# Performance work log

Measured on AMD Instinct MI355X. Metric: run time of the kernel, lower is better.

The kernel has to match this reference:

```python
import jax, jax.numpy as jnp
import numpy as np

B, D_IN, D_Z, D_H, D_T, D_REC = 8192, 1024, 256, 256, 16, 256


def _softplus_beta(x, beta):
    # torch F.softplus(x, beta) = (1/beta) * log(1 + exp(beta*x))
    return jax.nn.softplus(beta * x) / beta


def setup_inputs() -> dict:
    key = jax.random.key(0)
    ks = jax.random.split(key, 17)
    w = lambda k, o, i: jax.random.normal(k, (o, i), jnp.float32) * (1.0 / np.sqrt(i))
    return {
        "I_t": jax.random.uniform(ks[0], (B, D_IN), jnp.float32),
        "h_m_1": jax.random.uniform(ks[1], (B, D_H), jnp.float32),
        "z_m_1": jax.random.uniform(ks[2], (B, D_Z), jnp.float32),
        "theta_m_1": jax.random.normal(ks[3], (B, D_T), jnp.float32),
        "eps_z": jax.random.normal(ks[4], (B, D_Z), jnp.float32),
        "eps_zhat": jax.random.normal(ks[5], (B, D_Z), jnp.float32),
        "W_post_mu": w(ks[6], D_Z, D_IN),
        "W_post_lv": w(ks[7], D_Z, D_IN),
        "W_z2h": w(ks[8], D_H, D_Z),
        "W_h2h": w(ks[9], D_H, D_H),
        "W_prior_mu": w(ks[10], D_Z, D_H),
        "W_prior_lv": w(ks[11], D_Z, D_H),
        "W_i2t": w(ks[12], D_T, D_IN),
        "W_vip2t": w(ks[13], D_T, D_Z),
        "W_t2z": w(ks[14], D_Z, D_T),
        "W_rec1": w(ks[15], D_REC, D_Z),
        "W_rec2": w(ks[16], D_IN, D_REC),
    }


def reference(I_t, h_m_1, z_m_1, theta_m_1, eps_z, eps_zhat,
              W_post_mu, W_post_lv, W_z2h, W_h2h, W_prior_mu, W_prior_lv,
              W_i2t, W_vip2t, W_t2z, W_rec1, W_rec2):
    relu = jax.nn.relu
    # prior pathway (perception_only=True branch)
    mu_p = relu(h_m_1 @ W_prior_mu.T)                       # [B, D_Z]
    sigma_p = _softplus_beta(h_m_1 @ W_prior_lv.T, 1.2)     # [B, D_Z]
    # theta dynamics; vip_to_theta has Positive parametrization -> relu(W)
    theta_h = (0.5 * theta_m_1 + 0.1 * (I_t @ W_i2t.T)
               - jax.lax.stop_gradient(sigma_p) @ relu(W_vip2t).T)  # [B, D_T]
    theta = 0.001 * _softplus_beta(theta_h, 0.5)
    # posterior + reparameterized sample
    mu_q = relu(I_t @ W_post_mu.T)
    sigma_q = relu(I_t @ W_post_lv.T)
    raw_z = jnp.clip(mu_q + eps_z * sigma_q, 0.0, 1.0)
    thresholds = 10.0 * (theta @ relu(W_t2z).T)             # Positive parametrization
    z = relu(raw_z - thresholds)                            # [B, D_Z]
    # reconstruction (two bias-free linears + sigmoid)
    I_hat = jax.nn.sigmoid((z @ W_rec1.T) @ W_rec2.T)       # [B, D_IN]
    # higher-state update and prior sample
    h = relu(z_m_1 @ W_z2h.T + h_m_1 @ W_h2h.T)             # [B, D_H]
    z_hat = mu_p + eps_zhat * sigma_p                       # [B, D_Z]
    # losses (as in torch forward)
    spatial = jnp.mean((I_t - I_hat) ** 2)
    temporal = jnp.mean((jax.lax.stop_gradient(z) - z_hat) ** 2)
    energy = jnp.mean(jnp.abs(z))
    return (I_hat, z, h, z_hat, spatial, temporal, energy)
```

## Files before the change

### kernel.cpp

```cpp
#include <hip/hip_runtime.h>
#include <math.h>

#define BB 8192
#define DIN 1024
#define DZ 256
#define DH 256
#define DT 16
#define DREC 256

#define OFF_IHAT 0
#define OFF_Z    (BB * DIN)
#define OFF_H    (OFF_Z + BB * DZ)
#define OFF_ZHAT (OFF_H + BB * DH)
#define OFF_SCAL (OFF_ZHAT + BB * DZ)

#define WS_HBF   0
#define WS_ZM1   2097152
#define WS_W     4194304
#define W_PM  (WS_W + 0)
#define W_PL  (W_PM + 262144)
#define W_Z2H (W_PL + 262144)
#define W_H2H (W_Z2H + 65536)
#define W_PRM (W_H2H + 65536)
#define W_PRL (W_PRM + 65536)
#define W_I2T (W_PRL + 65536)
#define W_VIP (W_I2T + 16384)
#define W_R1  (W_VIP + 4096)
#define W_R2  (W_R1 + 65536)
#define WS_ENDW  (W_R2 + 262144)
#define WS_SIGMA WS_ENDW
#define WS_ZBF   (WS_SIGMA + 2097152)
#define WS_R1BF  (WS_ZBF + 2097152)

typedef unsigned short u16;
typedef __attribute__((ext_vector_type(8))) unsigned short u16x8;
typedef __attribute__((ext_vector_type(8))) __bf16 bf16x8;
typedef __attribute__((ext_vector_type(4))) float f32x4;

#define MFMA __builtin_amdgcn_mfma_f32_16x16x32_bf16

__device__ inline u16 f2bf(float f) {
  unsigned u = __builtin_bit_cast(unsigned, f);
  u += 0x7fff + ((u >> 16) & 1);
  return (u16)(u >> 16);
}
__device__ inline float softplus_stable(float y) {
  return (y > 20.f) ? y : log1pf(expf(y));
}
__device__ inline bf16x8 gf(const u16* p) {
  return __builtin_bit_cast(bf16x8, *(const u16x8*)p);
}
__device__ inline f32x4 fzero() { return (f32x4){0.f, 0.f, 0.f, 0.f}; }

__device__ inline float block_sum256(float v, float* rbuf) {
#pragma unroll
  for (int off = 32; off > 0; off >>= 1) v += __shfl_down(v, off, 64);
  __syncthreads();
  if ((threadIdx.x & 63) == 0) rbuf[threadIdx.x >> 6] = v;
  __syncthreads();
  return rbuf[0] + rbuf[1] + rbuf[2] + rbuf[3];
}

__device__ inline void decode4(int id, int rows, int& row0, int& col0) {
  int xcd = id & 7, t = id >> 3;
  col0 = (t & 3) * 64;
  row0 = ((t >> 2) * 8 + xcd) * rows;
}

__device__ inline void dmaA32(u16* tile, const u16* __restrict__ gsrc,
                              int row0, int ldk, int k0) {
  const int lane = threadIdx.x & 63, w = threadIdx.x >> 6;
  int rb = w * 8;
  int r = rb + (lane >> 3);
  int gl = (lane & 7) ^ (r & 7);
  const u16* src = gsrc + (size_t)(row0 + r) * ldk + k0 + gl * 8;
  u16* dst = tile + rb * 64;
  __builtin_amdgcn_global_load_lds(
      (const __attribute__((address_space(1))) unsigned int*)(const void*)src,
      (__attribute__((address_space(3))) unsigned int*)(void*)dst, 16, 0, 0);
}
__device__ inline void dmaB64(u16* tile, const u16* __restrict__ gsrc,
                              int row0, int ldk, int k0) {
  const int lane = threadIdx.x & 63, w = threadIdx.x >> 6;
#pragma unroll
  for (int c = 0; c < 2; ++c) {
    int rb = w * 16 + c * 8;
    int r = rb + (lane >> 3);
    int gl = (lane & 7) ^ (r & 7);
    const u16* src = gsrc + (size_t)(row0 + r) * ldk + k0 + gl * 8;
    u16* dst = tile + rb * 64;
    __builtin_amdgcn_global_load_lds(
        (const __attribute__((address_space(1))) unsigned int*)(const void*)src,
        (__attribute__((address_space(3))) unsigned int*)(void*)dst, 16, 0, 0);
  }
}
__device__ inline void dma16(u16* tile, const u16* __restrict__ gsrc, int ldk,
                             int k0) {
  const int lane = threadIdx.x & 63, w = threadIdx.x >> 6;
  if (w < 2) {
    int rb = w * 8;
    int r = rb + (lane >> 3);
    int gl = (lane & 7) ^ (r & 7);
    const u16* src = gsrc + (size_t)r * ldk + k0 + gl * 8;
    u16* dst = tile + rb * 64;
    __builtin_amdgcn_global_load_lds(
        (const __attribute__((address_space(1))) unsigned int*)(const void*)src,
        (__attribute__((address_space(3))) unsigned int*)(void*)dst, 16, 0, 0);
  }
}
__device__ inline bf16x8 rd(const u16* tile, int r, int gl) {
  return gf(tile + r * 64 + ((gl ^ (r & 7)) * 8));
}

__global__ __launch_bounds__(256) void k_cvt(
    const float* __restrict__ I_t, const float* __restrict__ h_m_1,
    const float* __restrict__ z_m_1, const float* __restrict__ Wpm,
    const float* __restrict__ Wpl, const float* __restrict__ Wz2h,
    const float* __restrict__ Wh2h, const float* __restrict__ Wprm,
    const float* __restrict__ Wprl, const float* __restrict__ Wi2t,
    const float* __restrict__ Wv, const float* __restrict__ Wr1,
    const float* __restrict__ Wr2, u16* __restrict__ dstI,
    u16* __restrict__ dstW) {
  const int S1 = 8388608, S2 = 10485760, S3 = 12582912, S4 = 12845056,
            S5 = 13107200, S6 = 13172736, S7 = 13238272, S8 = 13303808,
            S9 = 13369344, S10 = 13385728, S11 = 13389824, S12 = 13455360,
            S13 = 13717504;
  int nchunk = S13 / 8;
  for (int c = blockIdx.x * 256 + threadIdx.x; c < nchunk;
       c += gridDim.x * 256) {
    int f = c * 8;
    const float* src;
    float scale = 1.f;
    bool nrelu = false;
    u16* dst;
    if (f < S1) {
      src = I_t + f;
      dst = dstI + f;
    } else {
      dst = dstW + (f - S1);
      if (f < S2)       src = h_m_1 + (f - S1);
      else if (f < S3)  src = z_m_1 + (f - S2);
      else if (f < S4)  src = Wpm + (f - S3);
      else if (f < S5)  src = Wpl + (f - S4);
      else if (f < S6)  src = Wz2h + (f - S5);
      else if (f < S7)  src = Wh2h + (f - S6);
      else if (f < S8)  src = Wprm + (f - S7);
      else if (f < S9)  src = Wprl + (f - S8);
      else if (f < S10) { src = Wi2t + (f - S9);  scale = 0.1f; }
      else if (f < S11) { src = Wv + (f - S10);   nrelu = true; }
      else if (f < S12) src = Wr1 + (f - S11);
      else              src = Wr2 + (f - S12);
    }
    float4 v0 = *(const float4*)(src);
    float4 v1 = *(const float4*)(src + 4);
    float vals[8] = {v0.x, v0.y, v0.z, v0.w, v1.x, v1.y, v1.z, v1.w};
    u16x8 o;
#pragma unroll
    for (int j = 0; j < 8; ++j) {
      float x = vals[j];
      x = nrelu ? -fmaxf(x, 0.f) : x * scale;
      o[j] = f2bf(x);
    }
    *(u16x8*)(dst) = o;
  }
}

__global__ __launch_bounds__(256, 4) void k_hp(
    const u16* __restrict__ h_bf, const u16* __restrict__ zm1,
    const u16* __restrict__ Wh2h, const u16* __restrict__ Wprm,
    const u16* __restrict__ Wprl, const u16* __restrict__ Wz2h,
    const float* __restrict__ eps_zhat, float* __restrict__ h_out,
    float* __restrict__ zhat_out, u16* __restrict__ sigma_bf) {
  __shared__ __align__(16) u16 smem[2048 + 3 * 4096];
  u16* As = smem;
  u16* B0s = smem + 2048;
  u16* B1s = B0s + 4096;
  u16* B2s = B1s + 4096;
  const int tid = threadIdx.x, lane = tid & 63, w = tid >> 6;
  const int frow = lane & 15, fq = lane >> 4;
  const int wr = w & 1, wc = w >> 1;
  int row0, col0;
  decode4(blockIdx.x, 32, row0, col0);

  f32x4 ah[2], am[2], as_[2];
#pragma unroll
  for (int i = 0; i < 2; ++i) { ah[i] = fzero(); am[i] = fzero(); as_[i] = fzero(); }

  for (int k0 = 0; k0 < DH; k0 += 64) {
    __syncthreads();
    dmaA32(As, h_bf, row0, DH, k0);
    dmaB64(B0s, Wh2h, col0, DH, k0);
    dmaB64(B1s, Wprm, col0, DH, k0);
    dmaB64(B2s, Wprl, col0, DH, k0);
    __syncthreads();
#pragma unroll
    for (int ks = 0; ks < 2; ++ks) {
      bf16x8 a = rd(As, wr * 16 + frow, ks * 4 + fq);
#pragma unroll
      for (int ni = 0; ni < 2; ++ni) {
        int br = wc * 32 + ni * 16 + frow;
        ah[ni]  = MFMA(a, rd(B0s, br, ks * 4 + fq), ah[ni], 0, 0, 0);
        am[ni]  = MFMA(a, rd(B1s, br, ks * 4 + fq), am[ni], 0, 0, 0);
        as_[ni] = MFMA(a, rd(B2s, br, ks * 4 + fq), as_[ni], 0, 0, 0);
      }
    }
  }
  for (int k0 = 0; k0 < DZ; k0 += 64) {
    __syncthreads();
    dmaA32(As, zm1, row0, DZ, k0);
    dmaB64(B0s, Wz2h, col0, DZ, k0);
    __syncthreads();
#pragma unroll
    for (int ks = 0; ks < 2; ++ks) {
      bf16x8 a = rd(As, wr * 16 + frow, ks * 4 + fq);
#pragma unroll
      for (int ni = 0; ni < 2; ++ni)
        ah[ni] = MFMA(a, rd(B0s, wc * 32 + ni * 16 + frow, ks * 4 + fq),
                      ah[ni], 0, 0, 0);
    }
  }
  __syncthreads();
  float* ht = (float*)smem;
  float* mt = (float*)(smem + 4224);
  float* st = (float*)(smem + 8448);
#pragma unroll
  for (int ni = 0; ni < 2; ++ni)
#pragma unroll
    for (int r = 0; r < 4; ++r) {
      int lr = wr * 16 + fq * 4 + r;
      int ln = wc * 32 + ni * 16 + frow;
      ht[lr * 66 + ln] = fmaxf(ah[ni][r], 0.f);
      mt[lr * 66 + ln] = fmaxf(am[ni][r], 0.f);
      st[lr * 66 + ln] = softplus_stable(1.2f * as_[ni][r]) * (1.f / 1.2f);
    }
  __syncthreads();
  {
    int lr2 = tid >> 3, c0 = (tid & 7) * 8;
    int m2 = row0 + lr2;
    float h8[8], mu8[8], sg8[8];
#pragma unroll
    for (int j = 0; j < 8; ++j) {
      h8[j] = ht[lr2 * 66 + c0 + j];
      mu8[j] = mt[lr2 * 66 + c0 + j];
      sg8[j] = st[lr2 * 66 + c0 + j];
    }
    float* hp = h_out + (size_t)m2 * DH + col0 + c0;
    *(float4*)hp = make_float4(h8[0], h8[1], h8[2], h8[3]);
    *(float4*)(hp + 4) = make_float4(h8[4], h8[5], h8[6], h8[7]);
    const float* ep = eps_zhat + (size_t)m2 * DZ + col0 + c0;
    float4 e0 = ((const float4*)ep)[0], e1 = ((const float4*)ep)[1];
    float e8[8] = {e0.x, e0.y, e0.z, e0.w, e1.x, e1.y, e1.z, e1.w};
    float zh8[8];
    u16x8 sb;
#pragma unroll
    for (int j = 0; j < 8; ++j) {
      zh8[j] = mu8[j] + e8[j] * sg8[j];
      sb[j] = f2bf(sg8[j]);
    }
    float* zp = zhat_out + (size_t)m2 * DZ + col0 + c0;
    *(float4*)zp = make_float4(zh8[0], zh8[1], zh8[2], zh8[3]);
    *(float4*)(zp + 4) = make_float4(zh8[4], zh8[5], zh8[6], zh8[7]);
    *(u16x8*)(sigma_bf + (size_t)m2 * DZ + col0 + c0) = sb;
  }
}

__global__ __launch_bounds__(256, 4) void k_post(
    const u16* __restrict__ I_bf, const u16* __restrict__ Wpm,
    const u16* __restrict__ Wpl, const u16* __restrict__ Wi2t,
    const u16* __restrict__ Wv, const u16* __restrict__ sigma_bf,
    const float* __restrict__ theta_m_1, const float* __restrict__ W_t2z,
    const float* __restrict__ eps_z, const float* __restrict__ zhat,
    float* __restrict__ z_out, u16* __restrict__ z_bf,
    float* __restrict__ scal) {
  __shared__ __align__(16) u16 smem[2048 + 4096 + 4096 + 1024];
  u16* As = smem;
  u16* B0s = smem + 2048;
  u16* B1s = B0s + 4096;
  u16* Bts = B1s + 4096;
  __shared__ float th_s[32 * 17];
  __shared__ float wt_s[64 * 17];
  __shared__ float rbuf[4];
  const int tid = threadIdx.x, lane = tid & 63, w = tid >> 6;
  const int frow = lane & 15, fq = lane >> 4;
  const int wr = w & 1, wc = w >> 1;
  int row0, col0;
  decode4(blockIdx.x, 32, row0, col0);

  f32x4 accm[2], accs[2], acct = fzero();
#pragma unroll
  for (int i = 0; i < 2; ++i) { accm[i] = fzero(); accs[i] = fzero(); }

  for (int k0 = 0; k0 < DIN; k0 += 64) {
    __syncthreads();
    dmaA32(As, I_bf, row0, DIN, k0);
    dmaB64(B0s, Wpm, col0, DIN, k0);
    dmaB64(B1s, Wpl, col0, DIN, k0);
    dma16(Bts, Wi2t, DIN, k0);
    __syncthreads();
#pragma unroll
    for (int ks = 0; ks < 2; ++ks) {
      bf16x8 a = rd(As, wr * 16 + frow, ks * 4 + fq);
#pragma unroll
      for (int ni = 0; ni < 2; ++ni) {
        int br = wc * 32 + ni * 16 + frow;
        accm[ni] = MFMA(a, rd(B0s, br, ks * 4 + fq), accm[ni], 0, 0, 0);
        accs[ni] = MFMA(a, rd(B1s, br, ks * 4 + fq), accs[ni], 0, 0, 0);
      }
      acct = MFMA(a, rd(Bts, frow, ks * 4 + fq), acct, 0, 0, 0);
    }
  }
  for (int k0 = 0; k0 < DZ; k0 += 64) {
    __syncthreads();
    dmaA32(As, sigma_bf, row0, DZ, k0);
    dma16(Bts, Wv, DZ, k0);
    __syncthreads();
#pragma unroll
    for (int ks = 0; ks < 2; ++ks)
      acct = MFMA(rd(As, wr * 16 + frow, ks * 4 + fq),
                  rd(Bts, frow, ks * 4 + fq), acct, 0, 0, 0);
  }
  __syncthreads();
  if (wc == 0) {
#pragma unroll
    for (int r = 0; r < 4; ++r) {
      int lr = wr * 16 + fq * 4 + r;
      float th = 0.5f * theta_m_1[(size_t)(row0 + lr) * DT + frow] + acct[r];
      th_s[lr * 17 + frow] = 0.002f * softplus_stable(0.5f * th);
    }
  }
  for (int idx = tid; idx < 64 * 16; idx += 256) {
    int n = idx >> 4, j = idx & 15;
    wt_s[n * 17 + j] = 10.f * fmaxf(W_t2z[(col0 + n) * DT + j], 0.f);
  }
  __syncthreads();
  float* zt = (float*)B0s;
#pragma unroll
  for (int ni = 0; ni < 2; ++ni)
#pragma unroll
    for (int r = 0; r < 4; ++r) {
      int lr = wr * 16 + fq * 4 + r;
      int ln = wc * 32 + ni * 16 + frow;
      int m = row0 + lr;
      float mu = fmaxf(accm[ni][r], 0.f);
      float sq = fmaxf(accs[ni][r], 0.f);
      float raw = mu + eps_z[(size_t)m * DZ + col0 + ln] * sq;
      raw = fminf(fmaxf(raw, 0.f), 1.f);
      float thr = 0.f;
#pragma unroll
      for (int j = 0; j < 16; ++j)
        thr = fmaf(th_s[lr * 17 + j], wt_s[ln * 17 + j], thr);
      zt[lr * 66 + ln] = fmaxf(raw - thr, 0.f);
    }
  __syncthreads();
  float tsum = 0.f, esum = 0.f;
  {
    int lr2 = tid >> 3, c0 = (tid & 7) * 8;
    int m2 = row0 + lr2;
    float z8[8];
#pragma unroll
    for (int j = 0; j < 8; ++j) z8[j] = zt[lr2 * 66 + c0 + j];
    float* zp = z_out + (size_t)m2 * DZ + col0 + c0;
    *(float4*)zp = make_float4(z8[0], z8[1], z8[2], z8[3]);
    *(float4*)(zp + 4) = make_float4(z8[4], z8[5], z8[6], z8[7]);
    u16x8 zb;
#pragma unroll
    for (int j = 0; j < 8; ++j) zb[j] = f2bf(z8[j]);
    *(u16x8*)(z_bf + (size_t)m2 * DZ + col0 + c0) = zb;
    const float* zhp = zhat + (size_t)m2 * DZ + col0 + c0;
    float4 h0 = ((const float4*)zhp)[0], h1 = ((const float4*)zhp)[1];
    float zh8[8] = {h0.x, h0.y, h0.z, h0.w, h1.x, h1.y, h1.z, h1.w};
#pragma unroll
    for (int j = 0; j < 8; ++j) {
      float d = z8[j] - zh8[j];
      tsum += d * d;
      esum += z8[j];
    }
  }
  float t = block_sum256(tsum, rbuf);
  if (tid == 0) atomicAdd(scal + 1, t * (1.f / ((float)BB * DZ)));
  float e = block_sum256(esum, rbuf);
  if (tid == 0) atomicAdd(scal + 2, e * (1.f / ((float)BB * DZ)));
}

__global__ __launch_bounds__(256, 4) void k_rec1(const u16* __restrict__ z_bf,
                                                 const u16* __restrict__ Wr1,
                                                 u16* __restrict__ r1_bf) {
  __shared__ __align__(16) u16 smem[2048 + 4096];
  u16* As = smem;
  u16* B0s = smem + 2048;
  const int tid = threadIdx.x, lane = tid & 63, w = tid >> 6;
  const int frow = lane & 15, fq = lane >> 4;
  const int wr = w & 1, wc = w >> 1;
  int row0, col0;
  decode4(blockIdx.x, 32, row0, col0);
  f32x4 acc[2] = {fzero(), fzero()};
  for (int k0 = 0; k0 < DZ; k0 += 64) {
    __syncthreads();
    dmaA32(As, z_bf, row0, DZ, k0);
    dmaB64(B0s, Wr1, col0, DZ, k0);
    __syncthreads();
#pragma unroll
    for (int ks = 0; ks < 2; ++ks) {
      bf16x8 a = rd(As, wr * 16 + frow, ks * 4 + fq);
#pragma unroll
      for (int ni = 0; ni < 2; ++ni)
        acc[ni] = MFMA(a, rd(B0s, wc * 32 + ni * 16 + frow, ks * 4 + fq),
                       acc[ni], 0, 0, 0);
    }
  }
  __syncthreads();
  float* rt = (float*)smem;
#pragma unroll
  for (int ni = 0; ni < 2; ++ni)
#pragma unroll
    for (int r = 0; r < 4; ++r) {
      int lr = wr * 16 + fq * 4 + r;
      int ln = wc * 32 + ni * 16 + frow;
      rt[lr * 66 + ln] = acc[ni][r];
    }
  __syncthreads();
  {
    int lr2 = tid >> 3, c0 = (tid & 7) * 8;
    int m2 = row0 + lr2;
    u16x8 rb;
#pragma unroll
    for (int j = 0; j < 8; ++j) rb[j] = f2bf(rt[lr2 * 66 + c0 + j]);
    *(u16x8*)(r1_bf + (size_t)m2 * DREC + col0 + c0) = rb;
  }
}

__global__ __launch_bounds__(256, 4) void k_rec2(const u16* __restrict__ r1_bf,
                                                 const u16* __restrict__ Wr2,
                                                 const float* __restrict__ I_t,
                                                 float* __restrict__ ihat_out,
                                                 float* __restrict__ scal) {
  __shared__ __align__(16) u16 smem[4096 + 4096];
  u16* As = smem;
  u16* B0s = smem + 4096;
  __shared__ float rbuf[4];
  const int tid = threadIdx.x, lane = tid & 63, w = tid >> 6;
  const int frow = lane & 15, fq = lane >> 4;
  int row0, col0;
  {
    int id = blockIdx.x;
    int xcd = id & 7, t = id >> 3;
    col0 = (t & 15) * 64;
    row0 = ((t >> 4) * 8 + xcd) * 64;
  }
  f32x4 acc[4] = {fzero(), fzero(), fzero(), fzero()};
  for (int k0 = 0; k0 < DREC; k0 += 64) {
    __syncthreads();
    dmaB64(As, r1_bf, row0, DREC, k0);
    dmaB64(B0s, Wr2, col0, DREC, k0);
    __syncthreads();
#pragma unroll
    for (int ks = 0; ks < 2; ++ks) {
      bf16x8 a = rd(As, w * 16 + frow, ks * 4 + fq);
#pragma unroll
      for (int ni = 0; ni < 4; ++ni)
        acc[ni] = MFMA(a, rd(B0s, ni * 16 + frow, ks * 4 + fq), acc[ni], 0, 0, 0);
    }
  }
  float lsum = 0.f;
  float* it = (float*)smem;
#pragma unroll 1
  for (int p = 0; p < 2; ++p) {
    __syncthreads();
    if ((w >> 1) == p) {
#pragma unroll
      for (int ni = 0; ni < 4; ++ni)
#pragma unroll
        for (int r = 0; r < 4; ++r) {
          int lrl = (w & 1) * 16 + fq * 4 + r;
          int ln = ni * 16 + frow;
          it[lrl * 66 + ln] = 1.f / (1.f + expf(-acc[ni][r]));
        }
    }
    __syncthreads();
    int lr2 = tid >> 3, c0 = (tid & 7) * 8;
    int m2 = row0 + p * 32 + lr2;
    float i8[8];
#pragma unroll
    for (int j = 0; j < 8; ++j) i8[j] = it[lr2 * 66 + c0 + j];
    float* op = ihat_out + (size_t)m2 * DIN + col0 + c0;
    *(float4*)op = make_float4(i8[0], i8[1], i8[2], i8[3]);
    *(float4*)(op + 4) = make_float4(i8[4], i8[5], i8[6], i8[7]);
    const float* ip = I_t + (size_t)m2 * DIN + col0 + c0;
    float4 a0 = ((const float4*)ip)[0], a1 = ((const float4*)ip)[1];
    float t8[8] = {a0.x, a0.y, a0.z, a0.w, a1.x, a1.y, a1.z, a1.w};
#pragma unroll
    for (int j = 0; j < 8; ++j) {
      float d = t8[j] - i8[j];
      lsum += d * d;
    }
  }
  float s = block_sum256(lsum, rbuf);
  if (tid == 0) atomicAdd(scal + 0, s * (1.f / ((float)BB * DIN)));
}

extern "C" void kernel_launch(void* const* d_in, const int* in_sizes, int n_in,
                              void* d_out, int out_size, void* d_ws,
                              size_t ws_size, hipStream_t stream) {
  const float* I_t       = (const float*)d_in[0];
  const float* h_m_1     = (const float*)d_in[1];
  const float* z_m_1     = (const float*)d_in[2];
  const float* theta_m_1 = (const float*)d_in[3];
  const float* eps_z     = (const float*)d_in[4];
  const float* eps_zhat  = (const float*)d_in[5];
  const float* W_post_mu = (const float*)d_in[6];
  const float* W_post_lv = (const float*)d_in[7];
  const float* W_z2h     = (const float*)d_in[8];
  const float* W_h2h     = (const float*)d_in[9];
  const float* W_prior_mu= (const float*)d_in[10];
  const float* W_prior_lv= (const float*)d_in[11];
  const float* W_i2t     = (const float*)d_in[12];
  const float* W_vip2t   = (const float*)d_in[13];
  const float* W_t2z     = (const float*)d_in[14];
  const float* W_rec1    = (const float*)d_in[15];
  const float* W_rec2    = (const float*)d_in[16];

  float* out = (float*)d_out;
  float* ihat = out + OFF_IHAT;
  float* zout = out + OFF_Z;
  float* hout = out + OFF_H;
  float* zhat = out + OFF_ZHAT;
  float* scal = out + OFF_SCAL;

  u16* ws_u = (u16*)d_ws;
  u16* I_bf = (u16*)ihat;
  u16* h_bf = ws_u + WS_HBF;
  u16* zm1_bf = ws_u + WS_ZM1;
  u16* sigma_bf = ws_u + WS_SIGMA;
  u16* z_bf = ws_u + WS_ZBF;
  u16* r1_bf = ws_u + WS_R1BF;

  hipMemsetAsync(scal, 0, 3 * sizeof(float), stream);

  k_cvt<<<2048, 256, 0, stream>>>(I_t, h_m_1, z_m_1, W_post_mu, W_post_lv,
                                  W_z2h, W_h2h, W_prior_mu, W_prior_lv, W_i2t,
                                  W_vip2t, W_rec1, W_rec2, I_bf, ws_u + WS_HBF);

  k_hp<<<1024, 256, 0, stream>>>(h_bf, zm1_bf, ws_u + W_H2H, ws_u + W_PRM,
                                 ws_u + W_PRL, ws_u + W_Z2H, eps_zhat, hout,
                                 zhat, sigma_bf);
  k_post<<<1024, 256, 0, stream>>>(I_bf, ws_u + W_PM, ws_u + W_PL,
                                   ws_u + W_I2T, ws_u + W_VIP, sigma_bf,
                                   theta_m_1, W_t2z, eps_z, zhat, zout, z_bf,
                                   scal);
  k_rec1<<<1024, 256, 0, stream>>>(z_bf, ws_u + W_R1, r1_bf);
  k_rec2<<<2048, 256, 0, stream>>>(r1_bf, ws_u + W_R2, I_t, ihat, scal);
}
```

Before: 248.1 us.

## Double-buffer LDS tiles with async prefetch in all GEMM kernels

Converts the K-loops of k_hp, k_post, k_rec1 and k_rec2 from load-then-compute with two full barriers into a ping-pong LDS scheme. The next tile's DMA is issued before computing on the current one, and partial vmcnt waits are used so global loads overlap with MFMA work. This doubles shared memory per block, which may reduce occupancy. It also relies on hand-counted vmcnt values matching the number of loads each DMA helper issues, which is fragile.

```diff
diff --git a/kernel.cpp b/kernel.cpp
--- a/kernel.cpp
+++ b/kernel.cpp
@@ -38,6 +38,11 @@
 typedef __attribute__((ext_vector_type(4))) float f32x4;
 
 #define MFMA __builtin_amdgcn_mfma_f32_16x16x32_bf16
+
+#define VMW(n) asm volatile("s_waitcnt vmcnt(" #n ")" ::: "memory")
+#define LGK0() asm volatile("s_waitcnt lgkmcnt(0)" ::: "memory")
+#define SBAR() __builtin_amdgcn_s_barrier()
+#define SCH0() __builtin_amdgcn_sched_barrier(0)
 
 __device__ inline u16 f2bf(float f) {
   unsigned u = __builtin_bit_cast(unsigned, f);
@@ -171,11 +176,7 @@
     const u16* __restrict__ Wprl, const u16* __restrict__ Wz2h,
     const float* __restrict__ eps_zhat, float* __restrict__ h_out,
     float* __restrict__ zhat_out, u16* __restrict__ sigma_bf) {
-  __shared__ __align__(16) u16 smem[2048 + 3 * 4096];
-  u16* As = smem;
-  u16* B0s = smem + 2048;
-  u16* B1s = B0s + 4096;
-  u16* B2s = B1s + 4096;
+  __shared__ __align__(16) u16 smem[2 * 14336];
   const int tid = threadIdx.x, lane = tid & 63, w = tid >> 6;
   const int frow = lane & 15, fq = lane >> 4;
   const int wr = w & 1, wc = w >> 1;
@@ -186,38 +187,62 @@
 #pragma unroll
   for (int i = 0; i < 2; ++i) { ah[i] = fzero(); am[i] = fzero(); as_[i] = fzero(); }
 
-  for (int k0 = 0; k0 < DH; k0 += 64) {
-    __syncthreads();
-    dmaA32(As, h_bf, row0, DH, k0);
-    dmaB64(B0s, Wh2h, col0, DH, k0);
-    dmaB64(B1s, Wprm, col0, DH, k0);
-    dmaB64(B2s, Wprl, col0, DH, k0);
-    __syncthreads();
-#pragma unroll
-    for (int ks = 0; ks < 2; ++ks) {
-      bf16x8 a = rd(As, wr * 16 + frow, ks * 4 + fq);
-#pragma unroll
-      for (int ni = 0; ni < 2; ++ni) {
-        int br = wc * 32 + ni * 16 + frow;
-        ah[ni]  = MFMA(a, rd(B0s, br, ks * 4 + fq), ah[ni], 0, 0, 0);
-        am[ni]  = MFMA(a, rd(B1s, br, ks * 4 + fq), am[ni], 0, 0, 0);
-        as_[ni] = MFMA(a, rd(B2s, br, ks * 4 + fq), as_[ni], 0, 0, 0);
+  u16* cs = smem;
+  u16* ns = smem + 14336;
+  dmaA32(cs, h_bf, row0, DH, 0);
+  dmaB64(cs + 2048, Wh2h, col0, DH, 0);
+  dmaB64(cs + 6144, Wprm, col0, DH, 0);
+  dmaB64(cs + 10240, Wprl, col0, DH, 0);
+
+  for (int t = 0; t < 8; ++t) {
+    if (t < 7) {
+      int u = t + 1;
+      if (u < 4) {
+        int k0 = u * 64;
+        dmaA32(ns, h_bf, row0, DH, k0);
+        dmaB64(ns + 2048, Wh2h, col0, DH, k0);
+        dmaB64(ns + 6144, Wprm, col0, DH, k0);
+        dmaB64(ns + 10240, Wprl, col0, DH, k0);
+      } else {
+        int k0 = (u - 4) * 64;
+        dmaA32(ns, zm1, row0, DZ, k0);
+        dmaB64(ns + 2048, Wz2h, col0, DZ, k0);
       }
     }
-  }
-  for (int k0 = 0; k0 < DZ; k0 += 64) {
-    __syncthreads();
-    dmaA32(As, zm1, row0, DZ, k0);
-    dmaB64(B0s, Wz2h, col0, DZ, k0);
-    __syncthreads();
-#pragma unroll
-    for (int ks = 0; ks < 2; ++ks) {
-      bf16x8 a = rd(As, wr * 16 + frow, ks * 4 + fq);
-#pragma unroll
-      for (int ni = 0; ni < 2; ++ni)
-        ah[ni] = MFMA(a, rd(B0s, wc * 32 + ni * 16 + frow, ks * 4 + fq),
-                      ah[ni], 0, 0, 0);
-    }
+    if (t < 3) VMW(7);
+    else if (t < 7) VMW(3);
+    else VMW(0);
+    SBAR();
+    SCH0();
+    const u16* As = cs;
+    const u16* B0s = cs + 2048;
+    if (t < 4) {
+      const u16* B1s = cs + 6144;
+      const u16* B2s = cs + 10240;
+#pragma unroll
+      for (int ks = 0; ks < 2; ++ks) {
+        bf16x8 a = rd(As, wr * 16 + frow, ks * 4 + fq);
+#pragma unroll
+        for (int ni = 0; ni < 2; ++ni) {
+          int br = wc * 32 + ni * 16 + frow;
+          ah[ni]  = MFMA(a, rd(B0s, br, ks * 4 + fq), ah[ni], 0, 0, 0);
+          am[ni]  = MFMA(a, rd(B1s, br, ks * 4 + fq), am[ni], 0, 0, 0);
+          as_[ni] = MFMA(a, rd(B2s, br, ks * 4 + fq), as_[ni], 0, 0, 0);
+        }
+      }
+    } else {
+#pragma unroll
+      for (int ks = 0; ks < 2; ++ks) {
+        bf16x8 a = rd(As, wr * 16 + frow, ks * 4 + fq);
+#pragma unroll
+        for (int ni = 0; ni < 2; ++ni)
+          ah[ni] = MFMA(a, rd(B0s, wc * 32 + ni * 16 + frow, ks * 4 + fq),
+                        ah[ni], 0, 0, 0);
+      }
+    }
+    LGK0();
+    SBAR();
+    u16* tmp = cs; cs = ns; ns = tmp;
   }
   __syncthreads();
   float* ht = (float*)smem;
@@ -272,11 +297,7 @@
     const float* __restrict__ eps_z, const float* __restrict__ zhat,
     float* __restrict__ z_out, u16* __restrict__ z_bf,
     float* __restrict__ scal) {
-  __shared__ __align__(16) u16 smem[2048 + 4096 + 4096 + 1024];
-  u16* As = smem;
-  u16* B0s = smem + 2048;
-  u16* B1s = B0s + 4096;
-  u16* Bts = B1s + 4096;
+  __shared__ __align__(16) u16 smem[2 * 11264];
   __shared__ float th_s[32 * 17];
   __shared__ float wt_s[64 * 17];
   __shared__ float rbuf[4];
@@ -290,36 +311,59 @@
 #pragma unroll
   for (int i = 0; i < 2; ++i) { accm[i] = fzero(); accs[i] = fzero(); }
 
-  for (int k0 = 0; k0 < DIN; k0 += 64) {
-    __syncthreads();
-    dmaA32(As, I_bf, row0, DIN, k0);
-    dmaB64(B0s, Wpm, col0, DIN, k0);
-    dmaB64(B1s, Wpl, col0, DIN, k0);
-    dma16(Bts, Wi2t, DIN, k0);
-    __syncthreads();
-#pragma unroll
-    for (int ks = 0; ks < 2; ++ks) {
-      bf16x8 a = rd(As, wr * 16 + frow, ks * 4 + fq);
-#pragma unroll
-      for (int ni = 0; ni < 2; ++ni) {
-        int br = wc * 32 + ni * 16 + frow;
-        accm[ni] = MFMA(a, rd(B0s, br, ks * 4 + fq), accm[ni], 0, 0, 0);
-        accs[ni] = MFMA(a, rd(B1s, br, ks * 4 + fq), accs[ni], 0, 0, 0);
+  u16* cs = smem;
+  u16* ns = smem + 11264;
+  dmaA32(cs, I_bf, row0, DIN, 0);
+  dmaB64(cs + 2048, Wpm, col0, DIN, 0);
+  dmaB64(cs + 6144, Wpl, col0, DIN, 0);
+  dma16(cs + 10240, Wi2t, DIN, 0);
+
+  for (int t = 0; t < 20; ++t) {
+    if (t < 19) {
+      int u = t + 1;
+      if (u < 16) {
+        int k0 = u * 64;
+        dmaA32(ns, I_bf, row0, DIN, k0);
+        dmaB64(ns + 2048, Wpm, col0, DIN, k0);
+        dmaB64(ns + 6144, Wpl, col0, DIN, k0);
+        dma16(ns + 10240, Wi2t, DIN, k0);
+      } else {
+        int k0 = (u - 16) * 64;
+        dmaA32(ns, sigma_bf, row0, DZ, k0);
+        dma16(ns + 10240, Wv, DZ, k0);
       }
-      acct = MFMA(a, rd(Bts, frow, ks * 4 + fq), acct, 0, 0, 0);
-    }
-  }
-  for (int k0 = 0; k0 < DZ; k0 += 64) {
-    __syncthreads();
-    dmaA32(As, sigma_bf, row0, DZ, k0);
-    dma16(Bts, Wv, DZ, k0);
-    __syncthreads();
-#pragma unroll
-    for (int ks = 0; ks < 2; ++ks)
-      acct = MFMA(rd(As, wr * 16 + frow, ks * 4 + fq),
-                  rd(Bts, frow, ks * 4 + fq), acct, 0, 0, 0);
-  }
-  __syncthreads();
+    }
+    if (t < 15) { if (w < 2) VMW(6); else VMW(5); }
+    else if (t < 19) { if (w < 2) VMW(2); else VMW(1); }
+    else VMW(0);
+    SBAR();
+    SCH0();
+    const u16* As = cs;
+    const u16* Bts = cs + 10240;
+    if (t < 16) {
+      const u16* B0s = cs + 2048;
+      const u16* B1s = cs + 6144;
+#pragma unroll
+      for (int ks = 0; ks < 2; ++ks) {
+        bf16x8 a = rd(As, wr * 16 + frow, ks * 4 + fq);
+#pragma unroll
+        for (int ni = 0; ni < 2; ++ni) {
+          int br = wc * 32 + ni * 16 + frow;
+          accm[ni] = MFMA(a, rd(B0s, br, ks * 4 + fq), accm[ni], 0, 0, 0);
+          accs[ni] = MFMA(a, rd(B1s, br, ks * 4 + fq), accs[ni], 0, 0, 0);
+        }
+        acct = MFMA(a, rd(Bts, frow, ks * 4 + fq), acct, 0, 0, 0);
+      }
+    } else {
+#pragma unroll
+      for (int ks = 0; ks < 2; ++ks)
+        acct = MFMA(rd(As, wr * 16 + frow, ks * 4 + fq),
+                    rd(Bts, frow, ks * 4 + fq), acct, 0, 0, 0);
+    }
+    LGK0();
+    SBAR();
+    u16* tmp = cs; cs = ns; ns = tmp;
+  }
   if (wc == 0) {
 #pragma unroll
     for (int r = 0; r < 4; ++r) {
@@ -333,7 +377,7 @@
     wt_s[n * 17 + j] = 10.f * fmaxf(W_t2z[(col0 + n) * DT + j], 0.f);
   }
   __syncthreads();
-  float* zt = (float*)B0s;
+  float* zt = (float*)(smem + 2048);
 #pragma unroll
   for (int ni = 0; ni < 2; ++ni)
 #pragma unroll
@@ -385,20 +429,30 @@
 __global__ __launch_bounds__(256, 4) void k_rec1(const u16* __restrict__ z_bf,
                                                  const u16* __restrict__ Wr1,
                                                  u16* __restrict__ r1_bf) {
-  __shared__ __align__(16) u16 smem[2048 + 4096];
-  u16* As = smem;
-  u16* B0s = smem + 2048;
+  __shared__ __align__(16) u16 smem[2 * 6144];
   const int tid = threadIdx.x, lane = tid & 63, w = tid >> 6;
   const int frow = lane & 15, fq = lane >> 4;
   const int wr = w & 1, wc = w >> 1;
   int row0, col0;
   decode4(blockIdx.x, 32, row0, col0);
   f32x4 acc[2] = {fzero(), fzero()};
-  for (int k0 = 0; k0 < DZ; k0 += 64) {
-    __syncthreads();
-    dmaA32(As, z_bf, row0, DZ, k0);
-    dmaB64(B0s, Wr1, col0, DZ, k0);
-    __syncthreads();
+
+  u16* cs = smem;
+  u16* ns = smem + 6144;
+  dmaA32(cs, z_bf, row0, DZ, 0);
+  dmaB64(cs + 2048, Wr1, col0, DZ, 0);
+  for (int t = 0; t < 4; ++t) {
+    if (t < 3) {
+      int k0 = (t + 1) * 64;
+      dmaA32(ns, z_bf, row0, DZ, k0);
+      dmaB64(ns + 2048, Wr1, col0, DZ, k0);
+    }
+    if (t < 3) VMW(3);
+    else VMW(0);
+    SBAR();
+    SCH0();
+    const u16* As = cs;
+    const u16* B0s = cs + 2048;
 #pragma unroll
     for (int ks = 0; ks < 2; ++ks) {
       bf16x8 a = rd(As, wr * 16 + frow, ks * 4 + fq);
@@ -407,6 +461,9 @@
         acc[ni] = MFMA(a, rd(B0s, wc * 32 + ni * 16 + frow, ks * 4 + fq),
                        acc[ni], 0, 0, 0);
     }
+    LGK0();
+    SBAR();
+    u16* tmp = cs; cs = ns; ns = tmp;
   }
   __syncthreads();
   float* rt = (float*)smem;
@@ -434,9 +491,7 @@
                                                  const float* __restrict__ I_t,
                                                  float* __restrict__ ihat_out,
                                                  float* __restrict__ scal) {
-  __shared__ __align__(16) u16 smem[4096 + 4096];
-  u16* As = smem;
-  u16* B0s = smem + 4096;
+  __shared__ __align__(16) u16 smem[2 * 8192];
   __shared__ float rbuf[4];
   const int tid = threadIdx.x, lane = tid & 63, w = tid >> 6;
   const int frow = lane & 15, fq = lane >> 4;
@@ -448,11 +503,23 @@
     row0 = ((t >> 4) * 8 + xcd) * 64;
   }
   f32x4 acc[4] = {fzero(), fzero(), fzero(), fzero()};
-  for (int k0 = 0; k0 < DREC; k0 += 64) {
-    __syncthreads();
-    dmaB64(As, r1_bf, row0, DREC, k0);
-    dmaB64(B0s, Wr2, col0, DREC, k0);
-    __syncthreads();
+
+  u16* cs = smem;
+  u16* ns = smem + 8192;
+  dmaB64(cs, r1_bf, row0, DREC, 0);
+  dmaB64(cs + 4096, Wr2, col0, DREC, 0);
+  for (int t = 0; t < 4; ++t) {
+    if (t < 3) {
+      int k0 = (t + 1) * 64;
+      dmaB64(ns, r1_bf, row0, DREC, k0);
+      dmaB64(ns + 4096, Wr2, col0, DREC, k0);
+    }
+    if (t < 3) VMW(4);
+    else VMW(0);
+    SBAR();
+    SCH0();
+    const u16* As = cs;
+    const u16* B0s = cs + 4096;
 #pragma unroll
     for (int ks = 0; ks < 2; ++ks) {
       bf16x8 a = rd(As, w * 16 + frow, ks * 4 + fq);
@@ -460,6 +527,9 @@
       for (int ni = 0; ni < 4; ++ni)
         acc[ni] = MFMA(a, rd(B0s, ni * 16 + frow, ks * 4 + fq), acc[ni], 0, 0, 0);
     }
+    LGK0();
+    SBAR();
+    u16* tmp = cs; cs = ns; ns = tmp;
   }
   float lsum = 0.f;
   float* it = (float*)smem;
```

After: 260.1 us. 4.8% more time.

## Retile posterior kernel to 128-row blocks with register-held A and wide K windows

Applied to the files above, without the earlier changes.

The posterior GEMM kernel now uses 512-thread blocks covering 128 rows by 64 columns instead of 32x64. The weight tiles are staged 256 wide in K through LDS, while the input activations are loaded straight into registers per wave, so there are 4 K iterations instead of 16. This cuts the synchronisation count and reuses each weight tile across four times as many rows. The cost is a grid of only 256 blocks, which may underfill the GPU, plus higher LDS use per block and an epilogue restructured to compute thresholds per row.

```diff
diff --git a/kernel.cpp b/kernel.cpp
--- a/kernel.cpp
+++ b/kernel.cpp
@@ -60,6 +60,17 @@
   __syncthreads();
   return rbuf[0] + rbuf[1] + rbuf[2] + rbuf[3];
 }
+__device__ inline float block_sum512(float v, float* rbuf) {
+#pragma unroll
+  for (int off = 32; off > 0; off >>= 1) v += __shfl_down(v, off, 64);
+  __syncthreads();
+  if ((threadIdx.x & 63) == 0) rbuf[threadIdx.x >> 6] = v;
+  __syncthreads();
+  float s = 0.f;
+#pragma unroll
+  for (int i = 0; i < 8; ++i) s += rbuf[i];
+  return s;
+}
 
 __device__ inline void decode4(int id, int rows, int& row0, int& col0) {
   int xcd = id & 7, t = id >> 3;
@@ -94,22 +105,41 @@
         (__attribute__((address_space(3))) unsigned int*)(void*)dst, 16, 0, 0);
   }
 }
-__device__ inline void dma16(u16* tile, const u16* __restrict__ gsrc, int ldk,
-                             int k0) {
+__device__ inline bf16x8 rd(const u16* tile, int r, int gl) {
+  return gf(tile + r * 64 + ((gl ^ (r & 7)) * 8));
+}
+
+__device__ inline void stg64x256(u16* tile, const u16* __restrict__ g,
+                                 int row0, int ldk, int k0) {
   const int lane = threadIdx.x & 63, w = threadIdx.x >> 6;
-  if (w < 2) {
-    int rb = w * 8;
-    int r = rb + (lane >> 3);
-    int gl = (lane & 7) ^ (r & 7);
-    const u16* src = gsrc + (size_t)r * ldk + k0 + gl * 8;
-    u16* dst = tile + rb * 64;
+#pragma unroll
+  for (int i = 0; i < 4; ++i) {
+    int rb = (w * 4 + i) * 2;
+    int r = rb + (lane >> 5);
+    int d = lane & 31;
+    int s = d ^ (r & 7);
+    const u16* src = g + (size_t)(row0 + r) * ldk + k0 + s * 8;
+    u16* dst = tile + rb * 256;
     __builtin_amdgcn_global_load_lds(
         (const __attribute__((address_space(1))) unsigned int*)(const void*)src,
         (__attribute__((address_space(3))) unsigned int*)(void*)dst, 16, 0, 0);
   }
 }
-__device__ inline bf16x8 rd(const u16* tile, int r, int gl) {
-  return gf(tile + r * 64 + ((gl ^ (r & 7)) * 8));
+__device__ inline void stg16x256(u16* tile, const u16* __restrict__ g,
+                                 int ldk, int k0) {
+  const int lane = threadIdx.x & 63, w = threadIdx.x >> 6;
+  int rb = w * 2;
+  int r = rb + (lane >> 5);
+  int d = lane & 31;
+  int s = d ^ (r & 7);
+  const u16* src = g + (size_t)r * ldk + k0 + s * 8;
+  u16* dst = tile + rb * 256;
+  __builtin_amdgcn_global_load_lds(
+      (const __attribute__((address_space(1))) unsigned int*)(const void*)src,
+      (__attribute__((address_space(3))) unsigned int*)(void*)dst, 16, 0, 0);
+}
+__device__ inline bf16x8 rd256(const u16* tile, int r, int j) {
+  return gf(tile + r * 256 + ((j ^ (r & 7)) * 8));
 }
 
 __global__ __launch_bounds__(256) void k_cvt(
@@ -264,7 +294,7 @@
   }
 }
 
-__global__ __launch_bounds__(256, 4) void k_post(
+__global__ __launch_bounds__(512, 2) void k_post(
     const u16* __restrict__ I_bf, const u16* __restrict__ Wpm,
     const u16* __restrict__ Wpl, const u16* __restrict__ Wi2t,
     const u16* __restrict__ Wv, const u16* __restrict__ sigma_bf,
@@ -272,113 +302,135 @@
     const float* __restrict__ eps_z, const float* __restrict__ zhat,
     float* __restrict__ z_out, u16* __restrict__ z_bf,
     float* __restrict__ scal) {
-  __shared__ __align__(16) u16 smem[2048 + 4096 + 4096 + 1024];
-  u16* As = smem;
-  u16* B0s = smem + 2048;
-  u16* B1s = B0s + 4096;
-  u16* Bts = B1s + 4096;
-  __shared__ float th_s[32 * 17];
-  __shared__ float wt_s[64 * 17];
-  __shared__ float rbuf[4];
+  __shared__ __align__(16) u16 smem[36864];
+  __shared__ float thwt[128 * 17 + 64 * 17];
+  __shared__ float rbuf[8];
   const int tid = threadIdx.x, lane = tid & 63, w = tid >> 6;
   const int frow = lane & 15, fq = lane >> 4;
-  const int wr = w & 1, wc = w >> 1;
   int row0, col0;
-  decode4(blockIdx.x, 32, row0, col0);
-
-  f32x4 accm[2], accs[2], acct = fzero();
-#pragma unroll
-  for (int i = 0; i < 2; ++i) { accm[i] = fzero(); accs[i] = fzero(); }
-
-  for (int k0 = 0; k0 < DIN; k0 += 64) {
-    __syncthreads();
-    dmaA32(As, I_bf, row0, DIN, k0);
-    dmaB64(B0s, Wpm, col0, DIN, k0);
-    dmaB64(B1s, Wpl, col0, DIN, k0);
-    dma16(Bts, Wi2t, DIN, k0);
-    __syncthreads();
-#pragma unroll
-    for (int ks = 0; ks < 2; ++ks) {
-      bf16x8 a = rd(As, wr * 16 + frow, ks * 4 + fq);
-#pragma unroll
-      for (int ni = 0; ni < 2; ++ni) {
-        int br = wc * 32 + ni * 16 + frow;
-        accm[ni] = MFMA(a, rd(B0s, br, ks * 4 + fq), accm[ni], 0, 0, 0);
-        accs[ni] = MFMA(a, rd(B1s, br, ks * 4 + fq), accs[ni], 0, 0, 0);
+  {
+    int xcd = blockIdx.x & 7, t = blockIdx.x >> 3;
+    col0 = (t & 3) * 64;
+    row0 = ((t >> 2) * 8 + xcd) * 128;
+  }
+  u16* b0 = smem;
+
+  f32x4 mu[4], sg[4], tt = fzero();
+#pragma unroll
+  for (int i = 0; i < 4; ++i) { mu[i] = fzero(); sg[i] = fzero(); }
+
+  const u16* Abase = I_bf + (size_t)(row0 + w * 16 + frow) * DIN;
+  const u16* Sbase = sigma_bf + (size_t)(row0 + w * 16 + frow) * DZ;
+  bf16x8 ar[8];
+
+#pragma unroll 1
+  for (int p = 0; p < 4; ++p) {
+    int kwin = p * 256;
+    stg64x256(b0, Wpm, col0, DIN, kwin);
+    stg64x256(b0 + 16384, Wpl, col0, DIN, kwin);
+    stg16x256(b0 + 32768, Wi2t, DIN, kwin);
+#pragma unroll
+    for (int kk = 0; kk < 8; ++kk)
+      ar[kk] = gf(Abase + kwin + kk * 32 + fq * 8);
+    __syncthreads();
+#pragma unroll
+    for (int kk = 0; kk < 8; ++kk) {
+#pragma unroll
+      for (int n = 0; n < 4; ++n) {
+        mu[n] = MFMA(ar[kk], rd256(b0, n * 16 + frow, kk * 4 + fq),
+                     mu[n], 0, 0, 0);
+        sg[n] = MFMA(ar[kk], rd256(b0 + 16384, n * 16 + frow, kk * 4 + fq),
+                     sg[n], 0, 0, 0);
       }
-      acct = MFMA(a, rd(Bts, frow, ks * 4 + fq), acct, 0, 0, 0);
-    }
-  }
-  for (int k0 = 0; k0 < DZ; k0 += 64) {
-    __syncthreads();
-    dmaA32(As, sigma_bf, row0, DZ, k0);
-    dma16(Bts, Wv, DZ, k0);
-    __syncthreads();
-#pragma unroll
-    for (int ks = 0; ks < 2; ++ks)
-      acct = MFMA(rd(As, wr * 16 + frow, ks * 4 + fq),
-                  rd(Bts, frow, ks * 4 + fq), acct, 0, 0, 0);
-  }
-  __syncthreads();
-  if (wc == 0) {
-#pragma unroll
-    for (int r = 0; r < 4; ++r) {
-      int lr = wr * 16 + fq * 4 + r;
-      float th = 0.5f * theta_m_1[(size_t)(row0 + lr) * DT + frow] + acct[r];
-      th_s[lr * 17 + frow] = 0.002f * softplus_stable(0.5f * th);
-    }
-  }
-  for (int idx = tid; idx < 64 * 16; idx += 256) {
+      tt = MFMA(ar[kk], rd256(b0 + 32768, frow, kk * 4 + fq), tt, 0, 0, 0);
+    }
+    __syncthreads();
+  }
+  stg16x256(b0 + 32768, Wv, DZ, 0);
+#pragma unroll
+  for (int kk = 0; kk < 8; ++kk) ar[kk] = gf(Sbase + kk * 32 + fq * 8);
+  __syncthreads();
+#pragma unroll
+  for (int kk = 0; kk < 8; ++kk)
+    tt = MFMA(ar[kk], rd256(b0 + 32768, frow, kk * 4 + fq), tt, 0, 0, 0);
+  __syncthreads();
+
+  float* mt   = (float*)smem;
+  float* st   = (float*)(smem + 16896);
+  float* th_s = thwt;
+  float* wt_s = thwt + 128 * 17;
+
+#pragma unroll
+  for (int r = 0; r < 4; ++r) {
+    int lr = w * 16 + fq * 4 + r;
+    float th = 0.5f * theta_m_1[(size_t)(row0 + lr) * DT + frow] + tt[r];
+    th_s[lr * 17 + frow] = 0.002f * softplus_stable(0.5f * th);
+  }
+  for (int idx = tid; idx < 64 * 16; idx += 512) {
     int n = idx >> 4, j = idx & 15;
     wt_s[n * 17 + j] = 10.f * fmaxf(W_t2z[(col0 + n) * DT + j], 0.f);
   }
-  __syncthreads();
-  float* zt = (float*)B0s;
-#pragma unroll
-  for (int ni = 0; ni < 2; ++ni)
+#pragma unroll
+  for (int n = 0; n < 4; ++n)
 #pragma unroll
     for (int r = 0; r < 4; ++r) {
-      int lr = wr * 16 + fq * 4 + r;
-      int ln = wc * 32 + ni * 16 + frow;
-      int m = row0 + lr;
-      float mu = fmaxf(accm[ni][r], 0.f);
-      float sq = fmaxf(accs[ni][r], 0.f);
-      float raw = mu + eps_z[(size_t)m * DZ + col0 + ln] * sq;
-      raw = fminf(fmaxf(raw, 0.f), 1.f);
-      float thr = 0.f;
-#pragma unroll
-      for (int j = 0; j < 16; ++j)
-        thr = fmaf(th_s[lr * 17 + j], wt_s[ln * 17 + j], thr);
-      zt[lr * 66 + ln] = fmaxf(raw - thr, 0.f);
+      int lr = w * 16 + fq * 4 + r;
+      int ln = n * 16 + frow;
+      mt[lr * 66 + ln] = fmaxf(mu[n][r], 0.f);
+      st[lr * 66 + ln] = fmaxf(sg[n][r], 0.f);
     }
   __syncthreads();
   float tsum = 0.f, esum = 0.f;
   {
-    int lr2 = tid >> 3, c0 = (tid & 7) * 8;
+    int lr2 = tid >> 2, c0 = (tid & 3) * 16;
     int m2 = row0 + lr2;
-    float z8[8];
-#pragma unroll
-    for (int j = 0; j < 8; ++j) z8[j] = zt[lr2 * 66 + c0 + j];
-    float* zp = z_out + (size_t)m2 * DZ + col0 + c0;
-    *(float4*)zp = make_float4(z8[0], z8[1], z8[2], z8[3]);
-    *(float4*)(zp + 4) = make_float4(z8[4], z8[5], z8[6], z8[7]);
-    u16x8 zb;
-#pragma unroll
-    for (int j = 0; j < 8; ++j) zb[j] = f2bf(z8[j]);
-    *(u16x8*)(z_bf + (size_t)m2 * DZ + col0 + c0) = zb;
-    const float* zhp = zhat + (size_t)m2 * DZ + col0 + c0;
-    float4 h0 = ((const float4*)zhp)[0], h1 = ((const float4*)zhp)[1];
-    float zh8[8] = {h0.x, h0.y, h0.z, h0.w, h1.x, h1.y, h1.z, h1.w};
-#pragma unroll
-    for (int j = 0; j < 8; ++j) {
-      float d = z8[j] - zh8[j];
-      tsum += d * d;
-      esum += z8[j];
-    }
-  }
-  float t = block_sum256(tsum, rbuf);
+    float thv[16];
+#pragma unroll
+    for (int j = 0; j < 16; ++j) thv[j] = th_s[lr2 * 17 + j];
+#pragma unroll
+    for (int gb = 0; gb < 2; ++gb) {
+      int c = c0 + gb * 8;
+      float mu8[8], sg8[8];
+#pragma unroll
+      for (int j = 0; j < 8; ++j) {
+        mu8[j] = mt[lr2 * 66 + c + j];
+        sg8[j] = st[lr2 * 66 + c + j];
+      }
+      const float* ep = eps_z + (size_t)m2 * DZ + col0 + c;
+      float4 e0 = ((const float4*)ep)[0], e1 = ((const float4*)ep)[1];
+      float e8[8] = {e0.x, e0.y, e0.z, e0.w, e1.x, e1.y, e1.z, e1.w};
+      float z8[8];
+#pragma unroll
+      for (int j = 0; j < 8; ++j) {
+        float raw = mu8[j] + e8[j] * sg8[j];
+        raw = fminf(fmaxf(raw, 0.f), 1.f);
+        float thr = 0.f;
+#pragma unroll
+        for (int jj = 0; jj < 16; ++jj)
+          thr = fmaf(thv[jj], wt_s[(c + j) * 17 + jj], thr);
+        z8[j] = fmaxf(raw - thr, 0.f);
+      }
+      float* zp = z_out + (size_t)m2 * DZ + col0 + c;
+      *(float4*)zp = make_float4(z8[0], z8[1], z8[2], z8[3]);
+      *(float4*)(zp + 4) = make_float4(z8[4], z8[5], z8[6], z8[7]);
+      u16x8 zb;
+#pragma unroll
+      for (int j = 0; j < 8; ++j) zb[j] = f2bf(z8[j]);
+      *(u16x8*)(z_bf + (size_t)m2 * DZ + col0 + c) = zb;
+      const float* zhp = zhat + (size_t)m2 * DZ + col0 + c;
+      float4 h0 = ((const float4*)zhp)[0], h1 = ((const float4*)zhp)[1];
+      float zh8[8] = {h0.x, h0.y, h0.z, h0.w, h1.x, h1.y, h1.z, h1.w};
+#pragma unroll
+      for (int j = 0; j < 8; ++j) {
+        float d = z8[j] - zh8[j];
+        tsum += d * d;
+        esum += z8[j];
+      }
+    }
+  }
+  float t = block_sum512(tsum, rbuf);
   if (tid == 0) atomicAdd(scal + 1, t * (1.f / ((float)BB * DZ)));
-  float e = block_sum256(esum, rbuf);
+  float e = block_sum512(esum, rbuf);
   if (tid == 0) atomicAdd(scal + 2, e * (1.f / ((float)BB * DZ)));
 }
 
@@ -543,10 +595,10 @@
   k_hp<<<1024, 256, 0, stream>>>(h_bf, zm1_bf, ws_u + W_H2H, ws_u + W_PRM,
                                  ws_u + W_PRL, ws_u + W_Z2H, eps_zhat, hout,
                                  zhat, sigma_bf);
-  k_post<<<1024, 256, 0, stream>>>(I_bf, ws_u + W_PM, ws_u + W_PL,
-                                   ws_u + W_I2T, ws_u + W_VIP, sigma_bf,
-                                   theta_m_1, W_t2z, eps_z, zhat, zout, z_bf,
-                                   scal);
+  k_post<<<256, 512, 0, stream>>>(I_bf, ws_u + W_PM, ws_u + W_PL,
+                                  ws_u + W_I2T, ws_u + W_VIP, sigma_bf,
+                                  theta_m_1, W_t2z, eps_z, zhat, zout, z_bf,
+                                  scal);
   k_rec1<<<1024, 256, 0, stream>>>(z_bf, ws_u + W_R1, r1_bf);
   k_rec2<<<2048, 256, 0, stream>>>(r1_bf, ws_u + W_R2, I_t, ihat, scal);
 }
```

After: 238.3 us. -3.9%, faster.
